# Performance work log

Hardware: AMD Instinct MI355X
Metric: run time of the kernel (lower is better)

The kernel has to match this reference:

```python
import jax, jax.numpy as jnp
import numpy as np

POOL = 7  # fixed 7x7 output grid, hard-coded in the original layer


def _bin_bounds(step, rlen):
    # Replicates the original bin-corner logic + empty-bin adjustment.
    i = jnp.arange(POOL, dtype=jnp.int32)
    s = i * step
    e = jnp.where(i < POOL - 1, (i + 1) * step, rlen)
    empty = s == e
    # original: grow end by 1 if room, else shrink start by 1
    e = jnp.where(empty & (e < rlen), e + 1, e)
    s = jnp.where(empty & ~(e > (i * step)) , s, s)  # no-op placeholder for clarity
    s = jnp.where(empty & ((i * step) == e), (i * step) - 1, jnp.where(empty, i * step, s))
    # simpler equivalent: if still empty after trying to grow end, shrink start
    s0 = i * step
    e0 = jnp.where(i < POOL - 1, (i + 1) * step, rlen)
    grow = empty & (e0 < rlen)
    e = jnp.where(grow, e0 + 1, e0)
    s = jnp.where(empty & ~grow, s0 - 1, s0)
    return s, e


def _pool_one(roi, fm):
    # fm: [H, W, C]; roi: [4] normalized (y1, x1, y2, x2)
    H, W, C = fm.shape
    h0 = (H * roi[0]).astype(jnp.int32)  # tf.cast to int32 truncates (floor for >=0)
    w0 = (W * roi[1]).astype(jnp.int32)
    h1 = (H * roi[2]).astype(jnp.int32)
    w1 = (W * roi[3]).astype(jnp.int32)
    rh = h1 - h0
    rw = w1 - w0
    hstep = rh // POOL
    wstep = rw // POOL
    sh, eh = _bin_bounds(hstep, rh)  # [7], region-relative
    sw, ew = _bin_bounds(wstep, rw)
    hidx = jnp.arange(H, dtype=jnp.int32)
    widx = jnp.arange(W, dtype=jnp.int32)
    rmask = (hidx[None, :] >= (h0 + sh)[:, None]) & (hidx[None, :] < (h0 + eh)[:, None])  # [7,H]
    cmask = (widx[None, :] >= (w0 + sw)[:, None]) & (widx[None, :] < (w0 + ew)[:, None])  # [7,W]
    neg = jnp.asarray(-jnp.inf, fm.dtype)
    # max over rows for each of the 7 row-bins: [7, W, C]
    t = jnp.max(jnp.where(rmask[:, :, None, None], fm[None, :, :, :], neg), axis=1)
    # max over cols for each of the 7 col-bins: [7, 7, C]
    out = jnp.max(jnp.where(cmask[None, :, :, None], t[:, None, :, :], neg), axis=2)
    return out


def setup_inputs() -> dict:
    key = jax.random.key(0)
    k_f, k_y, k_x, k_h, k_w = jax.random.split(key, 5)
    H, W, C, N = 50, 50, 1024, 300
    features = jax.random.normal(k_f, (1, H, W, C), dtype=jnp.float32)
    # well-formed normalized ROIs: y1 < y2, x1 < x2, extent in [0.2, 0.55]
    y1 = jax.random.uniform(k_y, (N,), minval=0.0, maxval=0.45)
    x1 = jax.random.uniform(k_x, (N,), minval=0.0, maxval=0.45)
    hh = jax.random.uniform(k_h, (N,), minval=0.2, maxval=0.55)
    ww = jax.random.uniform(k_w, (N,), minval=0.2, maxval=0.55)
    rois = jnp.stack([y1, x1, jnp.minimum(y1 + hh, 1.0), jnp.minimum(x1 + ww, 1.0)], axis=1).astype(jnp.float32)
    return {"features": features, "rois": rois}


def reference(features, rois):
    fm = jnp.squeeze(features, axis=0)  # [H, W, C]
    # sequential over ROIs (mirrors tf.while_loop), fully vectorized per ROI
    pooled = jax.lax.map(lambda r: _pool_one(r, fm), rois)  # [N, 7, 7, C]
    return pooled
```

## Files before the change

### kernel.cpp

```cpp
#include <hip/hip_runtime.h>
#include <math.h>

#define POOL 7
#define FH 50
#define FW 50
#define FC 1024
#define FC4 (FC / 4)
#define CHUNKS 4
#define F4C 64

typedef float vf4 __attribute__((ext_vector_type(4)));

static __device__ __forceinline__ vf4 vmax4(vf4 a, vf4 b) {
    vf4 r;
    r.x = fmaxf(a.x, b.x);
    r.y = fmaxf(a.y, b.y);
    r.z = fmaxf(a.z, b.z);
    r.w = fmaxf(a.w, b.w);
    return r;
}

__global__ __launch_bounds__(256) void roipool_kernel(
    const float* __restrict__ fm,
    const float* __restrict__ rois,
    float* __restrict__ out,
    int nbins)
{
    const int b     = blockIdx.x;
    const int chunk = b & (CHUNKS - 1);
    const int wave  = threadIdx.x >> 6;
    const int lane  = threadIdx.x & 63;
    const int gid   = (b >> 2) * 4 + wave;
    if (gid >= nbins) return;

    const int n  = gid / 49;
    const int ij = gid - n * 49;
    const int i  = ij / 7;
    const int j  = ij - i * 7;

    const float4 roi = reinterpret_cast<const float4*>(rois)[n];
    const int h0 = (int)((float)FH * roi.x);
    const int w0 = (int)((float)FW * roi.y);
    const int h1 = (int)((float)FH * roi.z);
    const int w1 = (int)((float)FW * roi.w);
    const int rh = h1 - h0;
    const int rw = w1 - w0;
    const int hstep = rh / POOL;
    const int wstep = rw / POOL;

    int sh = i * hstep;
    int eh = (i < POOL - 1) ? (i + 1) * hstep : rh;
    if (sh == eh) { if (eh < rh) eh += 1; else sh -= 1; }
    int sw = j * wstep;
    int ew = (j < POOL - 1) ? (j + 1) * wstep : rw;
    if (sw == ew) { if (ew < rw) ew += 1; else sw -= 1; }

    const int r0 = max(0, h0 + sh);
    const int r1 = min(FH, h0 + eh);
    const int c0 = max(0, w0 + sw);
    const int c1 = min(FW, w0 + ew);

    const int f4 = chunk * F4C + lane;

    vf4 acc = {-INFINITY, -INFINITY, -INFINITY, -INFINITY};

    const vf4* fm4 = reinterpret_cast<const vf4*>(fm);

    for (int r = r0; r < r1; ++r) {
        const vf4* rowp = fm4 + (size_t)(r * FW) * FC4 + f4;
        int c = c0;
        for (; c + 1 < c1; c += 2) {
            vf4 a = rowp[(size_t)c * FC4];
            vf4 b2 = rowp[(size_t)(c + 1) * FC4];
            acc = vmax4(acc, vmax4(a, b2));
        }
        if (c < c1) {
            acc = vmax4(acc, rowp[(size_t)c * FC4]);
        }
    }

    vf4* o = reinterpret_cast<vf4*>(out) + (size_t)gid * FC4 + f4;
    __builtin_nontemporal_store(acc, o);
}

extern "C" void kernel_launch(void* const* d_in, const int* in_sizes, int n_in,
                              void* d_out, int out_size, void* d_ws, size_t ws_size,
                              hipStream_t stream) {
    const float* features = (const float*)d_in[0];
    const float* rois     = (const float*)d_in[1];
    float* out            = (float*)d_out;
    const int N = in_sizes[1] / 4;

    const int nbins = N * POOL * POOL;
    dim3 grid(((nbins + 3) / 4) * CHUNKS);
    dim3 block(256);
    roipool_kernel<<<grid, block, 0, stream>>>(features, rois, out, nbins);
}
```

Before: 96.71 us.

## Precompute 2x2 max-pooled pyramids to cut per-bin feature reads

Adds a build kernel that writes 2x1, 1x2 and 2x2 max-reduced copies of the feature map into the workspace. The pool kernel then covers the even-aligned interior of each bin with the 2x2 map and handles odd edges with the 1D maps or the raw map. This is meant to cut the number of vector loads per bin by about four. The cost is a second launch, extra workspace traffic, and more branching. The original single-pass kernel remains as a fallback when the workspace is too small.

```diff
diff --git a/kernel.cpp b/kernel.cpp
--- a/kernel.cpp
+++ b/kernel.cpp
@@ -8,6 +8,13 @@
 #define FC4 (FC / 4)
 #define CHUNKS 4
 #define F4C 64
+#define PH2 (FH / 2)
+#define PW2 (FW / 2)
+
+#define PW_OFF ((size_t)0)
+#define PH_OFF ((size_t)1250 * FC4)
+#define P2_OFF ((size_t)2500 * FC4)
+#define WS_VF4 ((size_t)3125 * FC4)
 
 typedef float vf4 __attribute__((ext_vector_type(4)));
 
@@ -20,25 +27,10 @@
     return r;
 }
 
-__global__ __launch_bounds__(256) void roipool_kernel(
-    const float* __restrict__ fm,
-    const float* __restrict__ rois,
-    float* __restrict__ out,
-    int nbins)
-{
-    const int b     = blockIdx.x;
-    const int chunk = b & (CHUNKS - 1);
-    const int wave  = threadIdx.x >> 6;
-    const int lane  = threadIdx.x & 63;
-    const int gid   = (b >> 2) * 4 + wave;
-    if (gid >= nbins) return;
-
-    const int n  = gid / 49;
-    const int ij = gid - n * 49;
-    const int i  = ij / 7;
-    const int j  = ij - i * 7;
-
-    const float4 roi = reinterpret_cast<const float4*>(rois)[n];
+static __device__ __forceinline__ void roi_bounds(
+    const float4 roi, int i, int j,
+    int& r0, int& r1, int& c0, int& c1)
+{
     const int h0 = (int)((float)FH * roi.x);
     const int w0 = (int)((float)FW * roi.y);
     const int h1 = (int)((float)FH * roi.z);
@@ -55,28 +47,166 @@
     int ew = (j < POOL - 1) ? (j + 1) * wstep : rw;
     if (sw == ew) { if (ew < rw) ew += 1; else sw -= 1; }
 
-    const int r0 = max(0, h0 + sh);
-    const int r1 = min(FH, h0 + eh);
-    const int c0 = max(0, w0 + sw);
-    const int c1 = min(FW, w0 + ew);
-
+    r0 = max(0, h0 + sh);
+    r1 = min(FH, h0 + eh);
+    c0 = max(0, w0 + sw);
+    c1 = min(FW, w0 + ew);
+}
+
+__global__ __launch_bounds__(256) void build_kernel(
+    const float* __restrict__ fm, float* __restrict__ ws)
+{
+    const int b     = blockIdx.x;
+    const int chunk = b & (CHUNKS - 1);
+    const int wave  = threadIdx.x >> 6;
+    const int lane  = threadIdx.x & 63;
+    const int s     = (b >> 2) * 4 + wave;
+    if (s >= PH2 * PW2) return;
+    const int rr = s / PW2;
+    const int cc = s - rr * PW2;
     const int f4 = chunk * F4C + lane;
 
+    const vf4* fm4 = reinterpret_cast<const vf4*>(fm);
+    const size_t rs = (size_t)FW * FC4;
+    const vf4* p = fm4 + (size_t)(2 * rr) * rs + (size_t)(2 * cc) * FC4 + f4;
+
+    vf4 a = p[0];
+    vf4 bb = p[FC4];
+    vf4 c = p[rs];
+    vf4 d = p[rs + FC4];
+
+    vf4 ab = vmax4(a, bb);
+    vf4 cd = vmax4(c, d);
+    vf4 ac = vmax4(a, c);
+    vf4 bd = vmax4(bb, d);
+
+    vf4* w4 = reinterpret_cast<vf4*>(ws);
+    w4[PW_OFF + ((size_t)(2 * rr) * PW2 + cc) * FC4 + f4]     = ab;
+    w4[PW_OFF + ((size_t)(2 * rr + 1) * PW2 + cc) * FC4 + f4] = cd;
+    w4[PH_OFF + ((size_t)rr * FW + 2 * cc) * FC4 + f4]        = ac;
+    w4[PH_OFF + ((size_t)rr * FW + 2 * cc + 1) * FC4 + f4]    = bd;
+    w4[P2_OFF + ((size_t)rr * PW2 + cc) * FC4 + f4]           = vmax4(ab, cd);
+}
+
+__global__ __launch_bounds__(256) void pool_kernel(
+    const float* __restrict__ fm,
+    const float* __restrict__ rois,
+    const float* __restrict__ ws,
+    float* __restrict__ out,
+    int nbins)
+{
+    const int b     = blockIdx.x;
+    const int chunk = b & (CHUNKS - 1);
+    const int wave  = threadIdx.x >> 6;
+    const int lane  = threadIdx.x & 63;
+    const int gid   = (b >> 2) * 4 + wave;
+    if (gid >= nbins) return;
+
+    const int n  = gid / 49;
+    const int ij = gid - n * 49;
+    const int i  = ij / 7;
+    const int j  = ij - i * 7;
+
+    const float4 roi = reinterpret_cast<const float4*>(rois)[n];
+    int r0, r1, c0, c1;
+    roi_bounds(roi, i, j, r0, r1, c0, c1);
+
+    int rA = r0 + (r0 & 1);
+    int rB = r1 & ~1;
+    int eR[2]; int nER = 0;
+    if (rA < rB) {
+        if (r0 < rA) eR[nER++] = r0;
+        if (rB < r1) eR[nER++] = rB;
+    } else {
+        for (int r = r0; r < r1; ++r) eR[nER++] = r;
+        rA = 0; rB = 0;
+    }
+    int cA = c0 + (c0 & 1);
+    int cB = c1 & ~1;
+    int eC[2]; int nEC = 0;
+    if (cA < cB) {
+        if (c0 < cA) eC[nEC++] = c0;
+        if (cB < c1) eC[nEC++] = cB;
+    } else {
+        for (int c = c0; c < c1; ++c) eC[nEC++] = c;
+        cA = 0; cB = 0;
+    }
+
+    const int f4 = chunk * F4C + lane;
     vf4 acc = {-INFINITY, -INFINITY, -INFINITY, -INFINITY};
 
+    const vf4* w4     = reinterpret_cast<const vf4*>(ws);
+    const vf4* p2base = w4 + P2_OFF + f4;
+    const vf4* phbase = w4 + PH_OFF + f4;
+    const vf4* pwbase = w4 + PW_OFF + f4;
+    const vf4* fmbase = reinterpret_cast<const vf4*>(fm) + f4;
+
+    for (int rp = rA; rp < rB; rp += 2) {
+        const vf4* row = p2base + (size_t)(rp >> 1) * PW2 * FC4;
+        int cp = cA;
+        for (; cp + 2 < cB; cp += 4) {
+            vf4 x = row[(size_t)(cp >> 1) * FC4];
+            vf4 y = row[(size_t)((cp >> 1) + 1) * FC4];
+            acc = vmax4(acc, vmax4(x, y));
+        }
+        if (cp < cB) acc = vmax4(acc, row[(size_t)(cp >> 1) * FC4]);
+    }
+    for (int rp = rA; rp < rB; rp += 2) {
+        const vf4* row = phbase + (size_t)(rp >> 1) * FW * FC4;
+        for (int k = 0; k < nEC; ++k)
+            acc = vmax4(acc, row[(size_t)eC[k] * FC4]);
+    }
+    for (int k = 0; k < nER; ++k) {
+        const vf4* row = pwbase + (size_t)eR[k] * PW2 * FC4;
+        for (int cp = cA; cp < cB; cp += 2)
+            acc = vmax4(acc, row[(size_t)(cp >> 1) * FC4]);
+    }
+    for (int k = 0; k < nER; ++k) {
+        const vf4* row = fmbase + (size_t)eR[k] * FW * FC4;
+        for (int m = 0; m < nEC; ++m)
+            acc = vmax4(acc, row[(size_t)eC[m] * FC4]);
+    }
+
+    vf4* o = reinterpret_cast<vf4*>(out) + (size_t)gid * FC4 + f4;
+    __builtin_nontemporal_store(acc, o);
+}
+
+__global__ __launch_bounds__(256) void roipool_direct_kernel(
+    const float* __restrict__ fm,
+    const float* __restrict__ rois,
+    float* __restrict__ out,
+    int nbins)
+{
+    const int b     = blockIdx.x;
+    const int chunk = b & (CHUNKS - 1);
+    const int wave  = threadIdx.x >> 6;
+    const int lane  = threadIdx.x & 63;
+    const int gid   = (b >> 2) * 4 + wave;
+    if (gid >= nbins) return;
+
+    const int n  = gid / 49;
+    const int ij = gid - n * 49;
+    const int i  = ij / 7;
+    const int j  = ij - i * 7;
+
+    const float4 roi = reinterpret_cast<const float4*>(rois)[n];
+    int r0, r1, c0, c1;
+    roi_bounds(roi, i, j, r0, r1, c0, c1);
+
+    const int f4 = chunk * F4C + lane;
+    vf4 acc = {-INFINITY, -INFINITY, -INFINITY, -INFINITY};
     const vf4* fm4 = reinterpret_cast<const vf4*>(fm);
+    const size_t rowstride = (size_t)FW * FC4;
 
     for (int r = r0; r < r1; ++r) {
-        const vf4* rowp = fm4 + (size_t)(r * FW) * FC4 + f4;
+        const vf4* rp0 = fm4 + (size_t)r * rowstride + f4;
         int c = c0;
         for (; c + 1 < c1; c += 2) {
-            vf4 a = rowp[(size_t)c * FC4];
-            vf4 b2 = rowp[(size_t)(c + 1) * FC4];
-            acc = vmax4(acc, vmax4(a, b2));
+            vf4 a0 = rp0[(size_t)c * FC4];
+            vf4 a1 = rp0[(size_t)(c + 1) * FC4];
+            acc = vmax4(acc, vmax4(a0, a1));
         }
-        if (c < c1) {
-            acc = vmax4(acc, rowp[(size_t)c * FC4]);
-        }
+        if (c < c1) acc = vmax4(acc, rp0[(size_t)c * FC4]);
     }
 
     vf4* o = reinterpret_cast<vf4*>(out) + (size_t)gid * FC4 + f4;
@@ -90,9 +220,20 @@
     const float* rois     = (const float*)d_in[1];
     float* out            = (float*)d_out;
     const int N = in_sizes[1] / 4;
-
     const int nbins = N * POOL * POOL;
-    dim3 grid(((nbins + 3) / 4) * CHUNKS);
-    dim3 block(256);
-    roipool_kernel<<<grid, block, 0, stream>>>(features, rois, out, nbins);
-}
+
+    const size_t ws_needed = WS_VF4 * sizeof(vf4);
+
+    if (ws_size >= ws_needed) {
+        const int nspatial = PH2 * PW2;
+        dim3 bgrid(((nspatial + 3) / 4) * CHUNKS);
+        build_kernel<<<bgrid, dim3(256), 0, stream>>>(features, (float*)d_ws);
+        dim3 pgrid(((nbins + 3) / 4) * CHUNKS);
+        pool_kernel<<<pgrid, dim3(256), 0, stream>>>(
+            features, rois, (const float*)d_ws, out, nbins);
+    } else {
+        dim3 grid(((nbins + 3) / 4) * CHUNKS);
+        roipool_direct_kernel<<<grid, dim3(256), 0, stream>>>(
+            features, rois, out, nbins);
+    }
+}
```

New measurement: 100.5 us. 3.9% more time.

## Process a full row-bin of seven column bins per wave instead of one bin

Applied to the files above, without the earlier changes.

Each wave now handles one ROI row-bin and all seven column bins, keeping seven accumulators in registers and walking each feature row once across the column ranges. The ROI and bin-bound arithmetic is shared across the seven outputs, and the grid is seven times smaller. Fewer waves exist to hide memory latency, and the inner loads become serial per column bin with a loop that is no longer unrolled by two, so parallelism and latency hiding may drop.

```diff
diff --git a/kernel.cpp b/kernel.cpp
--- a/kernel.cpp
+++ b/kernel.cpp
@@ -24,19 +24,17 @@
     const float* __restrict__ fm,
     const float* __restrict__ rois,
     float* __restrict__ out,
-    int nbins)
+    int nrb)
 {
     const int b     = blockIdx.x;
     const int chunk = b & (CHUNKS - 1);
     const int wave  = threadIdx.x >> 6;
     const int lane  = threadIdx.x & 63;
-    const int gid   = (b >> 2) * 4 + wave;
-    if (gid >= nbins) return;
+    const int t     = (b >> 2) * 4 + wave;
+    if (t >= nrb) return;
 
-    const int n  = gid / 49;
-    const int ij = gid - n * 49;
-    const int i  = ij / 7;
-    const int j  = ij - i * 7;
+    const int n = t / POOL;
+    const int i = t - n * POOL;
 
     const float4 roi = reinterpret_cast<const float4*>(rois)[n];
     const int h0 = (int)((float)FH * roi.x);
@@ -51,36 +49,42 @@
     int sh = i * hstep;
     int eh = (i < POOL - 1) ? (i + 1) * hstep : rh;
     if (sh == eh) { if (eh < rh) eh += 1; else sh -= 1; }
-    int sw = j * wstep;
-    int ew = (j < POOL - 1) ? (j + 1) * wstep : rw;
-    if (sw == ew) { if (ew < rw) ew += 1; else sw -= 1; }
-
     const int r0 = max(0, h0 + sh);
     const int r1 = min(FH, h0 + eh);
-    const int c0 = max(0, w0 + sw);
-    const int c1 = min(FW, w0 + ew);
+
+    int cs[POOL], ce[POOL];
+#pragma unroll
+    for (int j = 0; j < POOL; ++j) {
+        int sw = j * wstep;
+        int ew = (j < POOL - 1) ? (j + 1) * wstep : rw;
+        if (sw == ew) { if (ew < rw) ew += 1; else sw -= 1; }
+        cs[j] = max(0, w0 + sw);
+        ce[j] = min(FW, w0 + ew);
+    }
 
     const int f4 = chunk * F4C + lane;
 
-    vf4 acc = {-INFINITY, -INFINITY, -INFINITY, -INFINITY};
+    vf4 acc[POOL];
+#pragma unroll
+    for (int j = 0; j < POOL; ++j)
+        acc[j] = (vf4){-INFINITY, -INFINITY, -INFINITY, -INFINITY};
 
     const vf4* fm4 = reinterpret_cast<const vf4*>(fm);
+    const size_t rowstride = (size_t)FW * FC4;
 
     for (int r = r0; r < r1; ++r) {
-        const vf4* rowp = fm4 + (size_t)(r * FW) * FC4 + f4;
-        int c = c0;
-        for (; c + 1 < c1; c += 2) {
-            vf4 a = rowp[(size_t)c * FC4];
-            vf4 b2 = rowp[(size_t)(c + 1) * FC4];
-            acc = vmax4(acc, vmax4(a, b2));
-        }
-        if (c < c1) {
-            acc = vmax4(acc, rowp[(size_t)c * FC4]);
+        const vf4* rowp = fm4 + (size_t)r * rowstride + f4;
+#pragma unroll
+        for (int j = 0; j < POOL; ++j) {
+            for (int c = cs[j]; c < ce[j]; ++c)
+                acc[j] = vmax4(acc[j], rowp[(size_t)c * FC4]);
         }
     }
 
-    vf4* o = reinterpret_cast<vf4*>(out) + (size_t)gid * FC4 + f4;
-    __builtin_nontemporal_store(acc, o);
+    vf4* o = reinterpret_cast<vf4*>(out) + (size_t)(t * POOL) * FC4 + f4;
+#pragma unroll
+    for (int j = 0; j < POOL; ++j)
+        __builtin_nontemporal_store(acc[j], o + (size_t)j * FC4);
 }
 
 extern "C" void kernel_launch(void* const* d_in, const int* in_sizes, int n_in,
@@ -91,8 +95,8 @@
     float* out            = (float*)d_out;
     const int N = in_sizes[1] / 4;
 
-    const int nbins = N * POOL * POOL;
-    dim3 grid(((nbins + 3) / 4) * CHUNKS);
+    const int nrb = N * POOL;
+    dim3 grid(((nrb + 3) / 4) * CHUNKS);
     dim3 block(256);
-    roipool_kernel<<<grid, block, 0, stream>>>(features, rois, out, nbins);
+    roipool_kernel<<<grid, block, 0, stream>>>(features, rois, out, nrb);
 }
```

Result: slower. 127.7 us (+32.0%).
